# Performance work log

Hardware: AMD Instinct MI355X
Metric: run time of the kernel (lower is better)

## Reference

```python
import jax, jax.numpy as jnp
import numpy as np

K = 5
ALPHA = 0.5
TEMP = 10.0
EPS = 1e-12  # matches torch F.normalize default eps


def setup_inputs() -> dict:
    key = jax.random.key(0)
    k1, k2 = jax.random.split(key)
    embeddings = jax.random.normal(k1, (4, 2048, 2048), dtype=jnp.float32)
    vocab_embeddings = jax.random.normal(k2, (32000, 2048), dtype=jnp.float32)
    return {"embeddings": embeddings, "vocab_embeddings": vocab_embeddings}


def _l2_normalize(x):
    # torch.nn.functional.normalize: x / max(||x||, eps)
    n = jnp.linalg.norm(x, axis=-1, keepdims=True)
    return x / jnp.maximum(n, EPS)


def reference(embeddings, vocab_embeddings):
    B, S, D = embeddings.shape
    emb_flat = embeddings.reshape(-1, D)                      # [N, D]
    emb_n = _l2_normalize(emb_flat)
    voc_n = _l2_normalize(vocab_embeddings)                   # [V, D]
    sim = jnp.einsum('nd,vd->nv', emb_n, voc_n)               # [N, V]
    topk_sim, topk_idx = jax.lax.top_k(sim, K)                # [N, K]
    w = jax.nn.softmax(topk_sim * TEMP, axis=-1)              # [N, K]
    topk_emb = vocab_embeddings[topk_idx]                     # [N, K, D]
    projected = jnp.einsum('nk,nkd->nd', w, topk_emb)         # [N, D]
    result = ALPHA * emb_flat + (1.0 - ALPHA) * projected
    return result.reshape(B, S, D)
```

## Files before the change

kernel.cpp:

```cpp
#include <hip/hip_runtime.h>

typedef unsigned short u16;
typedef __attribute__((ext_vector_type(8))) short short8;
typedef __attribute__((ext_vector_type(4))) float float4v;

typedef __attribute__((address_space(3))) unsigned int lds_u32;
typedef __attribute__((address_space(1))) unsigned int glb_u32;

__device__ __forceinline__ void gld16(const void* g, void* l) {
    __builtin_amdgcn_global_load_lds((const glb_u32*)g, (lds_u32*)l, 16, 0, 0);
}

__device__ __forceinline__ u16 f2bf(float f) {
    union { float f; unsigned u; } x;
    x.f = f;
    unsigned r = x.u + 0x7FFFu + ((x.u >> 16) & 1u);
    return (u16)(r >> 16);
}

__device__ __forceinline__ u16 simkey(float v) {
    int k = (int)((v + 1.0f) * 32768.0f);
    k = k < 0 ? 0 : (k > 65535 ? 65535 : k);
    return (u16)k;
}

__global__ __launch_bounds__(256)
void rownorm_cast(const float* __restrict__ src, u16* __restrict__ dst,
                  double* __restrict__ invn)
{
    constexpr int D = 2048;
    __shared__ double red[256];
    __shared__ double invs;
    const int row = blockIdx.x;
    const int t = threadIdx.x;
    const float* sr = src + (size_t)row * D;
    float x[8];
    double ss = 0.0;
#pragma unroll
    for (int i = 0; i < 8; ++i) {
        x[i] = sr[t + i * 256];
        ss += (double)x[i] * (double)x[i];
    }
    red[t] = ss;
    __syncthreads();
    for (int s = 128; s > 0; s >>= 1) {
        if (t < s) red[t] += red[t + s];
        __syncthreads();
    }
    if (t == 0) {
        double n = sqrt(red[0]);
        double inv = 1.0 / fmax(n, 1e-12);
        invs = inv;
        invn[row] = inv;
    }
    __syncthreads();
    float inv = (float)invs;
    u16* dr = dst + (size_t)row * D;
#pragma unroll
    for (int i = 0; i < 8; ++i) dr[t + i * 256] = f2bf(x[i] * inv);
}

__global__ __launch_bounds__(256)
void rownorm_only(const float* __restrict__ src, double* __restrict__ invn,
                  float* __restrict__ invnf)
{
    constexpr int D = 2048;
    __shared__ double red[256];
    const int row = blockIdx.x;
    const int t = threadIdx.x;
    const float* sr = src + (size_t)row * D;
    double ss = 0.0;
#pragma unroll
    for (int i = 0; i < 8; ++i) {
        float v = sr[t + i * 256];
        ss += (double)v * (double)v;
    }
    red[t] = ss;
    __syncthreads();
    for (int s = 128; s > 0; s >>= 1) {
        if (t < s) red[t] += red[t + s];
        __syncthreads();
    }
    if (t == 0) {
        double n = sqrt(red[0]);
        double inv = 1.0 / fmax(n, 1e-12);
        invn[row] = inv;
        invnf[row] = (float)inv;
    }
}

__global__ __launch_bounds__(256)
void precast_rows(const float* __restrict__ Bf, const float* __restrict__ invBf,
                  u16* __restrict__ Bbf, int colBase)
{
    const int t = threadIdx.x;
    const int v = colBase + blockIdx.x;
    float s = invBf[v];
    const float* src = Bf + (size_t)v * 2048 + t * 8;
    float4v x0 = *(const float4v*)src;
    float4v x1 = *(const float4v*)(src + 4);
    short8 pk;
    pk[0] = (short)f2bf(x0[0] * s); pk[1] = (short)f2bf(x0[1] * s);
    pk[2] = (short)f2bf(x0[2] * s); pk[3] = (short)f2bf(x0[3] * s);
    pk[4] = (short)f2bf(x1[0] * s); pk[5] = (short)f2bf(x1[1] * s);
    pk[6] = (short)f2bf(x1[2] * s); pk[7] = (short)f2bf(x1[3] * s);
    *(short8*)(Bbf + (size_t)blockIdx.x * 2048 + t * 8) = pk;
}

__global__ __launch_bounds__(512, 2)
void gemm256_bt_u16(const u16* __restrict__ A, const u16* __restrict__ B,
                    u16* __restrict__ Csim, int ldc)
{
    constexpr int Kdim = 2048;
    constexpr int NT = Kdim / 64;
    __shared__ __align__(16) u16 As[2][256 * 64];
    __shared__ __align__(16) u16 Bs[2][192 * 64];
    const int tid = threadIdx.x;
    const int lane = tid & 63;
    const int wave = tid >> 6;
    const int bx = blockIdx.x & 31;
    const int by = blockIdx.x >> 5;
    const int rowTile = bx * 256;
    const int colTile = by * 192;
    const u16* Ab = A + (size_t)rowTile * Kdim;
    const u16* Bb = B + (size_t)colTile * Kdim;

    const int wr = (wave >> 2) * 128;
    const int wc = (wave & 3) * 48;
    const int lr = lane & 15;
    const int lq = lane >> 4;

    float4v acc[8][3];
#pragma unroll
    for (int i = 0; i < 8; ++i)
#pragma unroll
        for (int j = 0; j < 3; ++j) acc[i][j] = (float4v){0.f, 0.f, 0.f, 0.f};

    auto stage = [&](int t, int b) {
        int k0 = t * 64;
#pragma unroll
        for (int i = 0; i < 4; ++i) {
            int c = i * 512 + tid;
            int r = c >> 3, s = c & 7;
            gld16(Ab + (size_t)r * Kdim + k0 + ((s ^ (r & 7)) * 8), &As[b][c * 8]);
        }
#pragma unroll
        for (int i = 0; i < 3; ++i) {
            int c = i * 512 + tid;
            int r = c >> 3, s = c & 7;
            gld16(Bb + (size_t)r * Kdim + k0 + ((s ^ (r & 7)) * 8), &Bs[b][c * 8]);
        }
    };

    stage(0, 0);
    stage(1, 1);
    asm volatile("s_waitcnt vmcnt(7)" ::: "memory");
    __builtin_amdgcn_sched_barrier(0);
    __builtin_amdgcn_s_barrier();
    __builtin_amdgcn_sched_barrier(0);

    int cur = 0;
    for (int t = 0; t < NT; ++t) {
#pragma unroll
        for (int ks = 0; ks < 2; ++ks) {
            short8 af[8], bfr[3];
#pragma unroll
            for (int mi = 0; mi < 8; ++mi) {
                int r = wr + mi * 16 + lr;
                int s = (ks * 4 + lq) ^ (lr & 7);
                af[mi] = *(const short8*)&As[cur][r * 64 + s * 8];
            }
#pragma unroll
            for (int ni = 0; ni < 3; ++ni) {
                int r = wc + ni * 16 + lr;
                int s = (ks * 4 + lq) ^ (lr & 7);
                bfr[ni] = *(const short8*)&Bs[cur][r * 64 + s * 8];
            }
#pragma unroll
            for (int mi = 0; mi < 8; ++mi)
#pragma unroll
                for (int ni = 0; ni < 3; ++ni)
                    acc[mi][ni] = __builtin_amdgcn_mfma_f32_16x16x32_bf16(
                        af[mi], bfr[ni], acc[mi][ni], 0, 0, 0);
        }
        asm volatile("s_waitcnt lgkmcnt(0)" ::: "memory");
        __builtin_amdgcn_sched_barrier(0);
        __builtin_amdgcn_s_barrier();
        __builtin_amdgcn_sched_barrier(0);
        if (t + 2 < NT) {
            stage(t + 2, cur);
            asm volatile("s_waitcnt vmcnt(7)" ::: "memory");
        } else if (t + 1 < NT) {
            asm volatile("s_waitcnt vmcnt(0)" ::: "memory");
        }
        __builtin_amdgcn_sched_barrier(0);
        __builtin_amdgcn_s_barrier();
        __builtin_amdgcn_sched_barrier(0);
        cur ^= 1;
    }

#pragma unroll
    for (int mi = 0; mi < 8; ++mi) {
#pragma unroll
        for (int r = 0; r < 4; ++r) {
            int row = rowTile + wr + mi * 16 + lq * 4 + r;
            u16* crow = Csim + (size_t)row * ldc + colTile + wc + lr;
#pragma unroll
            for (int ni = 0; ni < 3; ++ni) crow[ni * 16] = simkey(acc[mi][ni][r]);
        }
    }
}

__global__ __launch_bounds__(256)
void top8_merge_u16(const u16* __restrict__ sims, int ldc, int cols, int colBase,
                    int* __restrict__ candK, int* __restrict__ candI, int isFirst,
                    const float* __restrict__ Bf, const float* __restrict__ invBf,
                    u16* __restrict__ Bbf, int nextBase, int nextCols)
{
    const int t = threadIdx.x;

    if (blockIdx.x < nextCols) {
        int v = nextBase + blockIdx.x;
        float s = invBf[v];
        const float* src = Bf + (size_t)v * 2048 + t * 8;
        float4v x0 = *(const float4v*)src;
        float4v x1 = *(const float4v*)(src + 4);
        short8 pks;
        pks[0] = (short)f2bf(x0[0] * s); pks[1] = (short)f2bf(x0[1] * s);
        pks[2] = (short)f2bf(x0[2] * s); pks[3] = (short)f2bf(x0[3] * s);
        pks[4] = (short)f2bf(x1[0] * s); pks[5] = (short)f2bf(x1[1] * s);
        pks[6] = (short)f2bf(x1[2] * s); pks[7] = (short)f2bf(x1[3] * s);
        *(short8*)(Bbf + (size_t)blockIdx.x * 2048 + t * 8) = pks;
    }

    const int lane = t & 63;
    const int wave = t >> 6;
    const int row = blockIdx.x * 4 + wave;
    const u16* srow = sims + (size_t)row * ldc;

    int pk[24];
#pragma unroll
    for (int i = 0; i < 3; ++i) {
        short8 v = *(const short8*)(srow + i * 512 + lane * 8);
#pragma unroll
        for (int e = 0; e < 8; ++e) {
            int j = i * 512 + lane * 8 + e;
            int key = (int)(u16)v[e];
            pk[i * 8 + e] = (j < cols) ? ((key << 11) | (2047 - j)) : -1;
        }
    }

    int best[8];
#pragma unroll
    for (int p = 0; p < 8; ++p) {
        int bv = -1;
#pragma unroll
        for (int i = 0; i < 24; ++i) bv = pk[i] > bv ? pk[i] : bv;
#pragma unroll
        for (int off = 32; off > 0; off >>= 1) {
            int ov = __shfl_xor(bv, off);
            bv = ov > bv ? ov : bv;
        }
        best[p] = bv;
        int cj = 2047 - (bv & 2047);
#pragma unroll
        for (int i = 0; i < 3; ++i)
#pragma unroll
            for (int e = 0; e < 8; ++e)
                if (i * 512 + lane * 8 + e == cj) pk[i * 8 + e] = -1;
    }

    if (lane == 0) {
        int bK[8], bI[8];
#pragma unroll
        for (int p = 0; p < 8; ++p) {
            bK[p] = best[p] >> 11;
            bI[p] = colBase + (2047 - (best[p] & 2047));
        }
        if (isFirst) {
            for (int i = 0; i < 8; ++i) {
                candK[row * 8 + i] = bK[i];
                candI[row * 8 + i] = bI[i];
            }
        } else {
            int oK[8], oI[8], nK[8], nI[8];
            for (int i = 0; i < 8; ++i) { oK[i] = candK[row * 8 + i]; oI[i] = candI[row * 8 + i]; }
            int a = 0, b = 0;
            for (int i = 0; i < 8; ++i) {
                if (oK[a] >= bK[b]) { nK[i] = oK[a]; nI[i] = oI[a]; ++a; }
                else { nK[i] = bK[b]; nI[i] = bI[b]; ++b; }
            }
            for (int i = 0; i < 8; ++i) { candK[row * 8 + i] = nK[i]; candI[row * 8 + i] = nI[i]; }
        }
    }
}

__global__ __launch_bounds__(256)
void finalize_kernel(const float* __restrict__ emb, const float* __restrict__ voc,
                     const double* __restrict__ invA, const double* __restrict__ invB,
                     const int* __restrict__ candI, float* __restrict__ out)
{
    constexpr int D = 2048;
    __shared__ float rows8[8][D];
    __shared__ float erow[D];
    __shared__ double wred[4][8];
    __shared__ double s8[8];
    __shared__ int i8[8];
    __shared__ float w5[5];
    __shared__ int slot5[5];
    const int row = blockIdx.x;
    const int t = threadIdx.x;
    const int lane = t & 63;
    const int wave = t >> 6;

    if (t < 8) i8[t] = candI[row * 8 + t];
    __syncthreads();
    {
        const float4v* er = (const float4v*)(emb + (size_t)row * D);
        float4v* ed = (float4v*)erow;
        ed[t] = er[t];
        ed[t + 256] = er[t + 256];
#pragma unroll
        for (int k = 0; k < 8; ++k) {
            const float4v* src = (const float4v*)(voc + (size_t)i8[k] * D);
            float4v* dst = (float4v*)rows8[k];
            dst[t] = src[t];
            dst[t + 256] = src[t + 256];
        }
    }
    __syncthreads();

    double part[8] = {0, 0, 0, 0, 0, 0, 0, 0};
#pragma unroll
    for (int i = 0; i < 8; ++i) {
        int d = t + i * 256;
        double e = (double)erow[d];
#pragma unroll
        for (int k = 0; k < 8; ++k) part[k] += e * (double)rows8[k][d];
    }
#pragma unroll
    for (int k = 0; k < 8; ++k) {
#pragma unroll
        for (int off = 32; off > 0; off >>= 1) part[k] += __shfl_down(part[k], off);
        if (lane == 0) wred[wave][k] = part[k];
    }
    __syncthreads();
    if (t < 8) {
        double sum = wred[0][t] + wred[1][t] + wred[2][t] + wred[3][t];
        s8[t] = sum * invA[row] * invB[i8[t]];
    }
    __syncthreads();
    if (t == 0) {
        int ord[8] = {0, 1, 2, 3, 4, 5, 6, 7};
        for (int a = 0; a < 5; ++a) {
            int best = a;
            for (int b = a + 1; b < 8; ++b) {
                if (s8[ord[b]] > s8[ord[best]] ||
                    (s8[ord[b]] == s8[ord[best]] && i8[ord[b]] < i8[ord[best]]))
                    best = b;
            }
            int tmp = ord[a]; ord[a] = ord[best]; ord[best] = tmp;
        }
        double m = s8[ord[0]];
        double e[5], sum = 0.0;
        for (int k = 0; k < 5; ++k) { e[k] = exp((s8[ord[k]] - m) * 10.0); sum += e[k]; }
        for (int k = 0; k < 5; ++k) {
            w5[k] = (float)(e[k] / sum);
            slot5[k] = ord[k];
        }
    }
    __syncthreads();
    float q0 = w5[0], q1 = w5[1], q2 = w5[2], q3 = w5[3], q4 = w5[4];
    int s0 = slot5[0], s1 = slot5[1], s2 = slot5[2], s3 = slot5[3], s4 = slot5[4];
    float* orow = out + (size_t)row * D;
#pragma unroll
    for (int i = 0; i < 8; ++i) {
        int d = t + i * 256;
        float p = q0 * rows8[s0][d] + q1 * rows8[s1][d] + q2 * rows8[s2][d] +
                  q3 * rows8[s3][d] + q4 * rows8[s4][d];
        orow[d] = 0.5f * erow[d] + 0.5f * p;
    }
}

extern "C" void kernel_launch(void* const* d_in, const int* in_sizes, int n_in,
                              void* d_out, int out_size, void* d_ws, size_t ws_size,
                              hipStream_t stream)
{
    (void)in_sizes; (void)n_in; (void)out_size; (void)ws_size;
    constexpr int N = 8192, V = 32000;
    constexpr int CHUNK = 1536;
    constexpr int NCHUNK = 21;
    const float* emb = (const float*)d_in[0];
    const float* voc = (const float*)d_in[1];
    float* out = (float*)d_out;
    char* ws = (char*)d_ws;

    double* invA  = (double*)(ws);
    double* invB  = (double*)(ws + 65536);
    float*  invBf = (float*)(ws + 321536);
    int*    candK = (int*)(ws + 449536);
    int*    candI = (int*)(ws + 711680);

    u16* Abf  = (u16*)d_out;
    u16* sims = (u16*)((char*)d_out + 33554432);
    u16* Bbf  = (u16*)((char*)d_out + 58720256);

    rownorm_cast<<<N, 256, 0, stream>>>(emb, Abf, invA);
    rownorm_only<<<V, 256, 0, stream>>>(voc, invB, invBf);
    precast_rows<<<CHUNK, 256, 0, stream>>>(voc, invBf, Bbf, 0);

    for (int c = 0; c < NCHUNK; ++c) {
        int colBase = c * CHUNK;
        int cols = (c == NCHUNK - 1) ? (V - colBase) : CHUNK;
        int nextBase = colBase + CHUNK;
        int nextCols = (c < NCHUNK - 1)
                           ? ((c + 1 == NCHUNK - 1) ? (V - nextBase) : CHUNK)
                           : 0;
        gemm256_bt_u16<<<dim3(256), 512, 0, stream>>>(Abf, Bbf, sims, CHUNK);
        top8_merge_u16<<<N / 4, 256, 0, stream>>>(sims, CHUNK, cols, colBase,
                                                  candK, candI, c == 0, voc,
                                                  invBf, Bbf, nextBase, nextCols);
    }

    finalize_kernel<<<N, 256, 0, stream>>>(emb, voc, invA, invB, candI, out);
}
```

Measured before the change: 2.231 ms.

## Triple-buffer A tiles and interleave prefetch with split MFMA phases

The bf16 GEMM main loop is split into four phases per K tile, each covering half the M fragments and one k-substep. One quarter of the next-next A tile is prefetched inside each phase, using a three-slot A buffer in LDS. Each phase is bracketed by barriers and raises wave priority with s_setprio around its MFMA block, so global loads and LDS reads spread across the loop instead of arriving in one burst. This aims to hide load latency and keep the matrix cores busier. The cost is more LDS (144KB per block) and four times as many workgroup barriers per tile.

```diff
diff --git a/kernel.cpp b/kernel.cpp
--- a/kernel.cpp
+++ b/kernel.cpp
@@ -113,7 +113,7 @@
 {
     constexpr int Kdim = 2048;
     constexpr int NT = Kdim / 64;
-    __shared__ __align__(16) u16 As[2][256 * 64];
+    __shared__ __align__(16) u16 As[3][256 * 64];
     __shared__ __align__(16) u16 Bs[2][192 * 64];
     const int tid = threadIdx.x;
     const int lane = tid & 63;
@@ -136,68 +136,90 @@
 #pragma unroll
         for (int j = 0; j < 3; ++j) acc[i][j] = (float4v){0.f, 0.f, 0.f, 0.f};
 
-    auto stage = [&](int t, int b) {
-        int k0 = t * 64;
-#pragma unroll
-        for (int i = 0; i < 4; ++i) {
-            int c = i * 512 + tid;
-            int r = c >> 3, s = c & 7;
-            gld16(Ab + (size_t)r * Kdim + k0 + ((s ^ (r & 7)) * 8), &As[b][c * 8]);
-        }
+    auto stageApiece = [&](int t2, int slot, int p) {
+        int c = p * 512 + tid;
+        int r = c >> 3, s = c & 7;
+        gld16(Ab + (size_t)r * Kdim + t2 * 64 + ((s ^ (r & 7)) * 8),
+              &As[slot][c * 8]);
+    };
+    auto stageB = [&](int t2, int b) {
 #pragma unroll
         for (int i = 0; i < 3; ++i) {
             int c = i * 512 + tid;
             int r = c >> 3, s = c & 7;
-            gld16(Bb + (size_t)r * Kdim + k0 + ((s ^ (r & 7)) * 8), &Bs[b][c * 8]);
+            gld16(Bb + (size_t)r * Kdim + t2 * 64 + ((s ^ (r & 7)) * 8),
+                  &Bs[b][c * 8]);
         }
     };
 
-    stage(0, 0);
-    stage(1, 1);
+#pragma unroll
+    for (int p = 0; p < 4; ++p) stageApiece(0, 0, p);
+    stageB(0, 0);
+#pragma unroll
+    for (int p = 0; p < 4; ++p) stageApiece(1, 1, p);
+    stageB(1, 1);
     asm volatile("s_waitcnt vmcnt(7)" ::: "memory");
     __builtin_amdgcn_sched_barrier(0);
     __builtin_amdgcn_s_barrier();
     __builtin_amdgcn_sched_barrier(0);
 
-    int cur = 0;
+#define PHASE(KS, MIH, PIECE, READ_B)                                          \
+    {                                                                          \
+        short8 af[4];                                                          \
+        _Pragma("unroll")                                                      \
+        for (int mi = 0; mi < 4; ++mi) {                                       \
+            int r = wr + ((MIH) * 4 + mi) * 16 + lr;                           \
+            int s = ((KS) * 4 + lq) ^ (lr & 7);                                \
+            af[mi] = *(const short8*)&Acur[r * 64 + s * 8];                    \
+        }                                                                      \
+        if (READ_B) {                                                          \
+            _Pragma("unroll")                                                  \
+            for (int ni = 0; ni < 3; ++ni) {                                   \
+                int r = wc + ni * 16 + lr;                                     \
+                int s = ((KS) * 4 + lq) ^ (lr & 7);                            \
+                bfr[ni] = *(const short8*)&Bcur[r * 64 + s * 8];               \
+            }                                                                  \
+        }                                                                      \
+        if (pf) stageApiece(t + 2, sA2, (PIECE));                              \
+        __builtin_amdgcn_s_barrier();                                          \
+        asm volatile("s_waitcnt lgkmcnt(0)" ::: "memory");                     \
+        __builtin_amdgcn_sched_barrier(0);                                     \
+        __builtin_amdgcn_s_setprio(1);                                         \
+        _Pragma("unroll")                                                      \
+        for (int mi = 0; mi < 4; ++mi)                                         \
+            _Pragma("unroll")                                                  \
+            for (int ni = 0; ni < 3; ++ni)                                     \
+                acc[(MIH) * 4 + mi][ni] =                                      \
+                    __builtin_amdgcn_mfma_f32_16x16x32_bf16(                   \
+                        af[mi], bfr[ni], acc[(MIH) * 4 + mi][ni], 0, 0, 0);    \
+        __builtin_amdgcn_s_setprio(0);                                         \
+        __builtin_amdgcn_s_barrier();                                          \
+        __builtin_amdgcn_sched_barrier(0);                                     \
+    }
+
     for (int t = 0; t < NT; ++t) {
-#pragma unroll
-        for (int ks = 0; ks < 2; ++ks) {
-            short8 af[8], bfr[3];
-#pragma unroll
-            for (int mi = 0; mi < 8; ++mi) {
-                int r = wr + mi * 16 + lr;
-                int s = (ks * 4 + lq) ^ (lr & 7);
-                af[mi] = *(const short8*)&As[cur][r * 64 + s * 8];
-            }
-#pragma unroll
-            for (int ni = 0; ni < 3; ++ni) {
-                int r = wc + ni * 16 + lr;
-                int s = (ks * 4 + lq) ^ (lr & 7);
-                bfr[ni] = *(const short8*)&Bs[cur][r * 64 + s * 8];
-            }
-#pragma unroll
-            for (int mi = 0; mi < 8; ++mi)
-#pragma unroll
-                for (int ni = 0; ni < 3; ++ni)
-                    acc[mi][ni] = __builtin_amdgcn_mfma_f32_16x16x32_bf16(
-                        af[mi], bfr[ni], acc[mi][ni], 0, 0, 0);
-        }
-        asm volatile("s_waitcnt lgkmcnt(0)" ::: "memory");
+        const u16* Acur = &As[t % 3][0];
+        const u16* Bcur = &Bs[t & 1][0];
+        const int sA2 = (t + 2) % 3;
+        const bool pf = (t + 2 < NT);
+        short8 bfr[3];
+
+        PHASE(0, 0, 0, 1)
+        PHASE(0, 1, 1, 0)
+        PHASE(1, 0, 2, 1)
+        PHASE(1, 1, 3, 0)
+
+        if (pf) {
+            stageB(t + 2, t & 1);
+            asm volatile("s_waitcnt vmcnt(7)" ::: "memory");
+        } else {
+            asm volatile("s_waitcnt vmcnt(0)" ::: "memory");
+        }
         __builtin_amdgcn_sched_barrier(0);
         __builtin_amdgcn_s_barrier();
         __builtin_amdgcn_sched_barrier(0);
-        if (t + 2 < NT) {
-            stage(t + 2, cur);
-            asm volatile("s_waitcnt vmcnt(7)" ::: "memory");
-        } else if (t + 1 < NT) {
-            asm volatile("s_waitcnt vmcnt(0)" ::: "memory");
-        }
-        __builtin_amdgcn_sched_barrier(0);
-        __builtin_amdgcn_s_barrier();
-        __builtin_amdgcn_sched_barrier(0);
-        cur ^= 1;
-    }
+    }
+#undef PHASE
 
 #pragma unroll
     for (int mi = 0; mi < 8; ++mi) {
```

Result: slower. 2.388 ms (+7.0%).
